# Kernel optimization log

Hardware: AMD Instinct MI355X
Metric: run time of the kernel (lower is better)

The kernel has to match this reference:

```python
import jax, jax.numpy as jnp
import numpy as np

B, S, I, H, C = 512, 512, 28, 128, 10


def setup_inputs() -> dict:
    key = jax.random.key(0)
    ks = jax.random.split(key, 11)
    std = 1.0 / np.sqrt(H)  # torch nn.RNN init scale
    u = lambda k, shape: jax.random.uniform(k, shape, jnp.float32, -std, std)
    return {
        "x": jax.random.normal(ks[0], (B, S, I), jnp.float32),
        "W_ih0": u(ks[1], (H, I)),
        "W_hh0": u(ks[2], (H, H)),
        "b_ih0": u(ks[3], (H,)),
        "b_hh0": u(ks[4], (H,)),
        "W_ih1": u(ks[5], (H, H)),
        "W_hh1": u(ks[6], (H, H)),
        "b_ih1": u(ks[7], (H,)),
        "b_hh1": u(ks[8], (H,)),
        "W_fc": u(ks[9], (C, H)),
        "b_fc": u(ks[10], (C,)),
    }


def reference(x, W_ih0, W_hh0, b_ih0, b_hh0, W_ih1, W_hh1, b_ih1, b_hh1, W_fc, b_fc):
    # 2-layer tanh RNN (batch_first); only the last timestep of layer 1 feeds fc,
    # so we carry hidden states through a scan without storing outputs.
    b = x.shape[0]
    h0_init = jnp.zeros((b, W_hh0.shape[0]), x.dtype)
    h1_init = jnp.zeros((b, W_hh1.shape[0]), x.dtype)

    def step(carry, xt):  # xt: [B, I]
        h0, h1 = carry
        h0 = jnp.tanh(xt @ W_ih0.T + b_ih0 + h0 @ W_hh0.T + b_hh0)
        h1 = jnp.tanh(h0 @ W_ih1.T + b_ih1 + h1 @ W_hh1.T + b_hh1)
        return (h0, h1), None

    xs = jnp.swapaxes(x, 0, 1)  # [S, B, I] time-major for scan
    (h0, h1), _ = jax.lax.scan(step, (h0_init, h1_init), xs)
    return h1 @ W_fc.T + b_fc  # [B, C]
```

## Files before the change

kernel.cpp:

```cpp
#include <hip/hip_runtime.h>

#define SEQ   512
#define IN    28
#define HID   128
#define NCLS  10
#define MB    16
#define PCH   144
#define MAGICF 12582912.0f

typedef __attribute__((ext_vector_type(4))) int   i32x4;
typedef __attribute__((ext_vector_type(4))) float f32x4;
typedef __attribute__((ext_vector_type(8))) short short8v;

#define SH_AA (1.0f/130048.0f)

__device__ __forceinline__ unsigned short f2bf(float f) {
    unsigned u = __float_as_uint(f);
    return (unsigned short)((u + 0x7FFFu + ((u >> 16) & 1u)) >> 16);
}
__device__ __forceinline__ float bf2f(unsigned short h) {
    return __uint_as_float(((unsigned)h) << 16);
}
__device__ __forceinline__ void split2(float f, unsigned short& hi, unsigned short& lo) {
    hi = f2bf(f);
    lo = f2bf(f - bf2f(hi));
}
__device__ __forceinline__ unsigned cvtpk(float a, float b) {
    unsigned r;
    asm("v_cvt_pk_bf16_f32 %0, %1, %2" : "=v"(r) : "v"(a), "v"(b));
    return r;
}
__device__ __forceinline__ float fast_tanh(float x) {
    float e = __expf(2.0f * x);
    return 1.0f - 2.0f * __builtin_amdgcn_rcpf(e + 1.0f);
}
__device__ __forceinline__ f32x4 mfma_bf(short8v a, short8v b, f32x4 c) {
    return __builtin_amdgcn_mfma_f32_16x16x32_bf16(a, b, c, 0, 0, 0);
}
__device__ __forceinline__ i32x4 mfma_i8(i32x4 a, i32x4 b, i32x4 c) {
    return __builtin_amdgcn_mfma_i32_16x16x64_i8(a, b, c, 0, 0, 0);
}
__device__ __forceinline__ void quantW(float wv, signed char& qa, signed char& qb) {
    int a = (int)rintf(wv * 1024.0f);
    float r = fmaf((float)a, -1.0f / 1024.0f, wv);
    int b = (int)rintf(r * 262144.0f);
    b = b > 127 ? 127 : (b < -127 ? -127 : b);
    qa = (signed char)a;
    qb = (signed char)b;
}
__device__ __forceinline__ unsigned quant4a(float t0, float t1, float t2, float t3) {
    unsigned u0 = __float_as_uint(fmaf(t0, 127.0f, MAGICF));
    unsigned u1 = __float_as_uint(fmaf(t1, 127.0f, MAGICF));
    unsigned u2 = __float_as_uint(fmaf(t2, 127.0f, MAGICF));
    unsigned u3 = __float_as_uint(fmaf(t3, 127.0f, MAGICF));
    return (u0 & 0xFFu) | ((u1 & 0xFFu) << 8) | ((u2 & 0xFFu) << 16) | ((u3 & 0xFFu) << 24);
}

union FragI8 { i32x4 v; signed char c[16]; };
union FragBF { short8v s; unsigned u[4]; };

__global__ __launch_bounds__(1024)
void rnn2_i8t(const float* __restrict__ x,
              const float* __restrict__ W_ih0, const float* __restrict__ W_hh0,
              const float* __restrict__ b_ih0, const float* __restrict__ b_hh0,
              const float* __restrict__ W_ih1, const float* __restrict__ W_hh1,
              const float* __restrict__ b_ih1, const float* __restrict__ b_hh1,
              const float* __restrict__ W_fc,  const float* __restrict__ b_fc,
              float* __restrict__ out)
{
    __shared__ __attribute__((aligned(16))) signed char hmem[2][2][MB * PCH];
    __shared__ float hfin[MB][HID + 4];

    const int t    = threadIdx.x;
    const int lane = t & 63;
    const int w    = t >> 6;
    const int lm   = lane & 15;
    const int lg   = lane >> 4;
    const int b0   = blockIdx.x * MB;
    const bool isL0 = (w < 8);
    const int T    = isL0 ? w : (w - 8);
    const int j    = 16 * T + lm;

    i32x4 Wa[2][2], Wb[2][2];
    short8v WxH = {}, WxL = {};
    float biasv[4];

    if (isL0) {
        #pragma unroll
        for (int kt = 0; kt < 2; ++kt) {
            const float* p = W_hh0 + j * HID + 64 * kt + 16 * lg;
            FragI8 a, b;
            #pragma unroll
            for (int e = 0; e < 16; ++e) quantW(p[e], a.c[e], b.c[e]);
            Wa[0][kt] = a.v; Wb[0][kt] = b.v;
        }
        FragBF H, L;
        #pragma unroll
        for (int p = 0; p < 4; ++p) {
            const int k0 = 8 * lg + 2 * p, k1 = k0 + 1;
            float w0 = (k0 < IN) ? W_ih0[j * IN + k0] : 0.0f;
            float w1 = (k1 < IN) ? W_ih0[j * IN + k1] : 0.0f;
            unsigned short h0s, l0s, h1s, l1s;
            split2(w0, h0s, l0s);
            split2(w1, h1s, l1s);
            H.u[p] = (unsigned)h0s | ((unsigned)h1s << 16);
            L.u[p] = (unsigned)l0s | ((unsigned)l1s << 16);
        }
        WxH = H.s; WxL = L.s;
        #pragma unroll
        for (int r = 0; r < 4; ++r) {
            const int u = 16 * T + 4 * lg + r;
            biasv[r] = b_ih0[u] + b_hh0[u];
        }
    } else {
        #pragma unroll
        for (int kt = 0; kt < 2; ++kt) {
            const float* p1 = W_ih1 + j * HID + 64 * kt + 16 * lg;
            const float* p2 = W_hh1 + j * HID + 64 * kt + 16 * lg;
            FragI8 a1, q1, a2, q2;
            #pragma unroll
            for (int e = 0; e < 16; ++e) {
                quantW(p1[e], a1.c[e], q1.c[e]);
                quantW(p2[e], a2.c[e], q2.c[e]);
            }
            Wa[0][kt] = a1.v; Wb[0][kt] = q1.v;
            Wa[1][kt] = a2.v; Wb[1][kt] = q2.v;
        }
        #pragma unroll
        for (int r = 0; r < 4; ++r) {
            const int u = 16 * T + 4 * lg + r;
            biasv[r] = b_ih1[u] + b_hh1[u];
        }
    }

    {
        int* z = (int*)&hmem[0][0][0];
        #pragma unroll
        for (int i = 0; i < 3; ++i) {
            const int idx = t + i * 1024;
            if (idx < (int)(sizeof(hmem) / 4)) z[idx] = 0;
        }
    }

    const float* xp = x + ((size_t)(b0 + lm) * SEQ) * IN + 8 * lg;
    float4 xA = make_float4(0.f, 0.f, 0.f, 0.f), xB = xA;
    if (isL0) {
        xA = *(const float4*)xp;
        if (lg < 3) xB = *(const float4*)(xp + 4);
    }
    __syncthreads();

    const int rbase = lm * PCH + 16 * lg;
    const int wbase = lm * PCH + 16 * T + 4 * lg;
    const i32x4 z4 = {0, 0, 0, 0};

    for (int it = 0; it <= SEQ; ++it) {
        const int rd = it & 1, wr = rd ^ 1;

        if (isL0) {
            i32x4 Ba0[2];
            Ba0[0] = *(const i32x4*)&hmem[0][rd][rbase];
            Ba0[1] = *(const i32x4*)&hmem[0][rd][rbase + 64];

            short8v BxH, BxL;
            {
                FragBF H, L;
                H.u[0] = cvtpk(xA.x, xA.y);
                H.u[1] = cvtpk(xA.z, xA.w);
                H.u[2] = cvtpk(xB.x, xB.y);
                H.u[3] = cvtpk(xB.z, xB.w);
                L.u[0] = cvtpk(xA.x - __uint_as_float(H.u[0] << 16),
                               xA.y - __uint_as_float(H.u[0] & 0xFFFF0000u));
                L.u[1] = cvtpk(xA.z - __uint_as_float(H.u[1] << 16),
                               xA.w - __uint_as_float(H.u[1] & 0xFFFF0000u));
                L.u[2] = cvtpk(xB.x - __uint_as_float(H.u[2] << 16),
                               xB.y - __uint_as_float(H.u[2] & 0xFFFF0000u));
                L.u[3] = cvtpk(xB.z - __uint_as_float(H.u[3] << 16),
                               xB.w - __uint_as_float(H.u[3] & 0xFFFF0000u));
                BxH = H.s; BxL = L.s;
            }
            {
                const int tn = (it < SEQ - 1) ? it + 1 : SEQ - 1;
                const float* p = xp + (size_t)tn * IN;
                xA = *(const float4*)p;
                xB = (lg < 3) ? *(const float4*)(p + 4) : make_float4(0.f, 0.f, 0.f, 0.f);
            }

            f32x4 accx = {biasv[0], biasv[1], biasv[2], biasv[3]};
            accx = mfma_bf(WxH, BxH, accx);
            accx = mfma_bf(WxL, BxH, accx);
            accx = mfma_bf(WxH, BxL, accx);

            i32x4 aa = mfma_i8(Wa[0][0], Ba0[0], z4);
            aa = mfma_i8(Wa[0][1], Ba0[1], aa);
            i32x4 cr = mfma_i8(Wb[0][0], Ba0[0], z4);
            cr = mfma_i8(Wb[0][1], Ba0[1], cr);

            float t0 = fast_tanh(accx[0] + SH_AA * fmaf((float)cr[0], 1.0f / 256.0f, (float)aa[0]));
            float t1 = fast_tanh(accx[1] + SH_AA * fmaf((float)cr[1], 1.0f / 256.0f, (float)aa[1]));
            float t2 = fast_tanh(accx[2] + SH_AA * fmaf((float)cr[2], 1.0f / 256.0f, (float)aa[2]));
            float t3 = fast_tanh(accx[3] + SH_AA * fmaf((float)cr[3], 1.0f / 256.0f, (float)aa[3]));
            *(unsigned*)&hmem[0][wr][wbase] = quant4a(t0, t1, t2, t3);
        } else {
            i32x4 Ba0[2], Ba1[2];
            Ba0[0] = *(const i32x4*)&hmem[0][rd][rbase];
            Ba0[1] = *(const i32x4*)&hmem[0][rd][rbase + 64];
            Ba1[0] = *(const i32x4*)&hmem[1][rd][rbase];
            Ba1[1] = *(const i32x4*)&hmem[1][rd][rbase + 64];

            i32x4 aa = mfma_i8(Wa[0][0], Ba0[0], z4);
            aa = mfma_i8(Wa[0][1], Ba0[1], aa);
            aa = mfma_i8(Wa[1][0], Ba1[0], aa);
            aa = mfma_i8(Wa[1][1], Ba1[1], aa);
            i32x4 cr = mfma_i8(Wb[0][0], Ba0[0], z4);
            cr = mfma_i8(Wb[0][1], Ba0[1], cr);
            cr = mfma_i8(Wb[1][0], Ba1[0], cr);
            cr = mfma_i8(Wb[1][1], Ba1[1], cr);

            float t0, t1, t2, t3;
            if (it == 0) {
                t0 = t1 = t2 = t3 = 0.0f;
            } else {
                t0 = fast_tanh(biasv[0] + SH_AA * fmaf((float)cr[0], 1.0f / 256.0f, (float)aa[0]));
                t1 = fast_tanh(biasv[1] + SH_AA * fmaf((float)cr[1], 1.0f / 256.0f, (float)aa[1]));
                t2 = fast_tanh(biasv[2] + SH_AA * fmaf((float)cr[2], 1.0f / 256.0f, (float)aa[2]));
                t3 = fast_tanh(biasv[3] + SH_AA * fmaf((float)cr[3], 1.0f / 256.0f, (float)aa[3]));
            }
            *(unsigned*)&hmem[1][wr][wbase] = quant4a(t0, t1, t2, t3);
            if (it == SEQ) {
                const int u = 16 * T + 4 * lg;
                hfin[lm][u + 0] = t0;
                hfin[lm][u + 1] = t1;
                hfin[lm][u + 2] = t2;
                hfin[lm][u + 3] = t3;
            }
        }
        __syncthreads();
    }

    if (t < MB * NCLS) {
        const int r = t / NCLS, c = t % NCLS;
        float acc = b_fc[c];
        const float* hf = &hfin[r][0];
        #pragma unroll 4
        for (int k = 0; k < HID; ++k)
            acc = fmaf(W_fc[c * HID + k], hf[k], acc);
        out[(b0 + r) * NCLS + c] = acc;
    }
}

extern "C" void kernel_launch(void* const* d_in, const int* in_sizes, int n_in,
                              void* d_out, int out_size, void* d_ws, size_t ws_size,
                              hipStream_t stream) {
    const float* x     = (const float*)d_in[0];
    const float* W_ih0 = (const float*)d_in[1];
    const float* W_hh0 = (const float*)d_in[2];
    const float* b_ih0 = (const float*)d_in[3];
    const float* b_hh0 = (const float*)d_in[4];
    const float* W_ih1 = (const float*)d_in[5];
    const float* W_hh1 = (const float*)d_in[6];
    const float* b_ih1 = (const float*)d_in[7];
    const float* b_hh1 = (const float*)d_in[8];
    const float* W_fc  = (const float*)d_in[9];
    const float* b_fc  = (const float*)d_in[10];
    float* out = (float*)d_out;

    rnn2_i8t<<<dim3(512 / MB), dim3(1024), 0, stream>>>(
        x, W_ih0, W_hh0, b_ih0, b_hh0, W_ih1, W_hh1, b_ih1, b_hh1, W_fc, b_fc, out);
}
```

Baseline: 329.4 us.

## Rebalance layer-1 waves to two tiles each and drop bf16 low-part input MFMAs

Layer 1 now runs on 4 waves that each compute two 16-row output tiles, so the block shrinks from 16 to 12 waves and per-wave layer-1 work matches layer-0's critical path more closely. The input projection keeps only the bf16 high part of x and W_ih0, removing two of three MFMAs and the split conversions. This trades input-projection precision for fewer instructions. Smaller tweaks fold the integer recombination into one shift-add plus fma, use exp2 in tanh, and pack bytes with v_perm.

Result: slower. 375.1 us (+13.9%).

```diff
diff --git a/kernel.cpp b/kernel.cpp
--- a/kernel.cpp
+++ b/kernel.cpp
@@ -12,18 +12,11 @@
 typedef __attribute__((ext_vector_type(4))) float f32x4;
 typedef __attribute__((ext_vector_type(8))) short short8v;
 
-#define SH_AA (1.0f/130048.0f)
+#define SH_CR (1.0f/33292288.0f)
 
 __device__ __forceinline__ unsigned short f2bf(float f) {
     unsigned u = __float_as_uint(f);
     return (unsigned short)((u + 0x7FFFu + ((u >> 16) & 1u)) >> 16);
-}
-__device__ __forceinline__ float bf2f(unsigned short h) {
-    return __uint_as_float(((unsigned)h) << 16);
-}
-__device__ __forceinline__ void split2(float f, unsigned short& hi, unsigned short& lo) {
-    hi = f2bf(f);
-    lo = f2bf(f - bf2f(hi));
 }
 __device__ __forceinline__ unsigned cvtpk(float a, float b) {
     unsigned r;
@@ -31,7 +24,7 @@
     return r;
 }
 __device__ __forceinline__ float fast_tanh(float x) {
-    float e = __expf(2.0f * x);
+    float e = exp2f(x * 2.8853900817779268f);
     return 1.0f - 2.0f * __builtin_amdgcn_rcpf(e + 1.0f);
 }
 __device__ __forceinline__ f32x4 mfma_bf(short8v a, short8v b, f32x4 c) {
@@ -53,14 +46,16 @@
     unsigned u1 = __float_as_uint(fmaf(t1, 127.0f, MAGICF));
     unsigned u2 = __float_as_uint(fmaf(t2, 127.0f, MAGICF));
     unsigned u3 = __float_as_uint(fmaf(t3, 127.0f, MAGICF));
-    return (u0 & 0xFFu) | ((u1 & 0xFFu) << 8) | ((u2 & 0xFFu) << 16) | ((u3 & 0xFFu) << 24);
+    unsigned t01 = __builtin_amdgcn_perm(u1, u0, 0x00000400u);
+    unsigned t23 = __builtin_amdgcn_perm(u3, u2, 0x00000400u);
+    return __builtin_amdgcn_perm(t23, t01, 0x05040100u);
 }
 
 union FragI8 { i32x4 v; signed char c[16]; };
 union FragBF { short8v s; unsigned u[4]; };
 
-__global__ __launch_bounds__(1024)
-void rnn2_i8t(const float* __restrict__ x,
+__global__ __launch_bounds__(768)
+void rnn2_i8w(const float* __restrict__ x,
               const float* __restrict__ W_ih0, const float* __restrict__ W_hh0,
               const float* __restrict__ b_ih0, const float* __restrict__ b_hh0,
               const float* __restrict__ W_ih1, const float* __restrict__ W_hh1,
@@ -78,14 +73,16 @@
     const int lg   = lane >> 4;
     const int b0   = blockIdx.x * MB;
     const bool isL0 = (w < 8);
-    const int T    = isL0 ? w : (w - 8);
-    const int j    = 16 * T + lm;
 
     i32x4 Wa[2][2], Wb[2][2];
-    short8v WxH = {}, WxL = {};
-    float biasv[4];
+    i32x4 W1a[2][2], W1b[2][2];
+    i32x4 W2a[2][2], W2b[2][2];
+    short8v WxH = {};
+    float bias0v[4];
+    float bias1v[2][4];
 
     if (isL0) {
+        const int j = 16 * w + lm;
         #pragma unroll
         for (int kt = 0; kt < 2; ++kt) {
             const float* p = W_hh0 + j * HID + 64 * kt + 16 * lg;
@@ -94,52 +91,51 @@
             for (int e = 0; e < 16; ++e) quantW(p[e], a.c[e], b.c[e]);
             Wa[0][kt] = a.v; Wb[0][kt] = b.v;
         }
-        FragBF H, L;
+        FragBF H;
         #pragma unroll
         for (int p = 0; p < 4; ++p) {
             const int k0 = 8 * lg + 2 * p, k1 = k0 + 1;
             float w0 = (k0 < IN) ? W_ih0[j * IN + k0] : 0.0f;
             float w1 = (k1 < IN) ? W_ih0[j * IN + k1] : 0.0f;
-            unsigned short h0s, l0s, h1s, l1s;
-            split2(w0, h0s, l0s);
-            split2(w1, h1s, l1s);
-            H.u[p] = (unsigned)h0s | ((unsigned)h1s << 16);
-            L.u[p] = (unsigned)l0s | ((unsigned)l1s << 16);
-        }
-        WxH = H.s; WxL = L.s;
+            H.u[p] = (unsigned)f2bf(w0) | ((unsigned)f2bf(w1) << 16);
+        }
+        WxH = H.s;
         #pragma unroll
         for (int r = 0; r < 4; ++r) {
-            const int u = 16 * T + 4 * lg + r;
-            biasv[r] = b_ih0[u] + b_hh0[u];
+            const int u = 16 * w + 4 * lg + r;
+            bias0v[r] = b_ih0[u] + b_hh0[u];
         }
     } else {
-        #pragma unroll
-        for (int kt = 0; kt < 2; ++kt) {
-            const float* p1 = W_ih1 + j * HID + 64 * kt + 16 * lg;
-            const float* p2 = W_hh1 + j * HID + 64 * kt + 16 * lg;
-            FragI8 a1, q1, a2, q2;
-            #pragma unroll
-            for (int e = 0; e < 16; ++e) {
-                quantW(p1[e], a1.c[e], q1.c[e]);
-                quantW(p2[e], a2.c[e], q2.c[e]);
-            }
-            Wa[0][kt] = a1.v; Wb[0][kt] = q1.v;
-            Wa[1][kt] = a2.v; Wb[1][kt] = q2.v;
-        }
-        #pragma unroll
-        for (int r = 0; r < 4; ++r) {
-            const int u = 16 * T + 4 * lg + r;
-            biasv[r] = b_ih1[u] + b_hh1[u];
+        const int w1 = w - 8;
+        #pragma unroll
+        for (int tile = 0; tile < 2; ++tile) {
+            const int T = 2 * w1 + tile;
+            const int j = 16 * T + lm;
+            #pragma unroll
+            for (int kt = 0; kt < 2; ++kt) {
+                const float* p1 = W_ih1 + j * HID + 64 * kt + 16 * lg;
+                const float* p2 = W_hh1 + j * HID + 64 * kt + 16 * lg;
+                FragI8 a1, q1, a2, q2;
+                #pragma unroll
+                for (int e = 0; e < 16; ++e) {
+                    quantW(p1[e], a1.c[e], q1.c[e]);
+                    quantW(p2[e], a2.c[e], q2.c[e]);
+                }
+                W1a[tile][kt] = a1.v; W1b[tile][kt] = q1.v;
+                W2a[tile][kt] = a2.v; W2b[tile][kt] = q2.v;
+            }
+            #pragma unroll
+            for (int r = 0; r < 4; ++r) {
+                const int u = 16 * T + 4 * lg + r;
+                bias1v[tile][r] = b_ih1[u] + b_hh1[u];
+            }
         }
     }
 
     {
         int* z = (int*)&hmem[0][0][0];
         #pragma unroll
-        for (int i = 0; i < 3; ++i) {
-            const int idx = t + i * 1024;
-            if (idx < (int)(sizeof(hmem) / 4)) z[idx] = 0;
-        }
+        for (int i = 0; i < 3; ++i) z[t + i * 768] = 0;
     }
 
     const float* xp = x + ((size_t)(b0 + lm) * SEQ) * IN + 8 * lg;
@@ -151,7 +147,6 @@
     __syncthreads();
 
     const int rbase = lm * PCH + 16 * lg;
-    const int wbase = lm * PCH + 16 * T + 4 * lg;
     const i32x4 z4 = {0, 0, 0, 0};
 
     for (int it = 0; it <= SEQ; ++it) {
@@ -162,23 +157,11 @@
             Ba0[0] = *(const i32x4*)&hmem[0][rd][rbase];
             Ba0[1] = *(const i32x4*)&hmem[0][rd][rbase + 64];
 
-            short8v BxH, BxL;
-            {
-                FragBF H, L;
-                H.u[0] = cvtpk(xA.x, xA.y);
-                H.u[1] = cvtpk(xA.z, xA.w);
-                H.u[2] = cvtpk(xB.x, xB.y);
-                H.u[3] = cvtpk(xB.z, xB.w);
-                L.u[0] = cvtpk(xA.x - __uint_as_float(H.u[0] << 16),
-                               xA.y - __uint_as_float(H.u[0] & 0xFFFF0000u));
-                L.u[1] = cvtpk(xA.z - __uint_as_float(H.u[1] << 16),
-                               xA.w - __uint_as_float(H.u[1] & 0xFFFF0000u));
-                L.u[2] = cvtpk(xB.x - __uint_as_float(H.u[2] << 16),
-                               xB.y - __uint_as_float(H.u[2] & 0xFFFF0000u));
-                L.u[3] = cvtpk(xB.z - __uint_as_float(H.u[3] << 16),
-                               xB.w - __uint_as_float(H.u[3] & 0xFFFF0000u));
-                BxH = H.s; BxL = L.s;
-            }
+            FragBF H;
+            H.u[0] = cvtpk(xA.x, xA.y);
+            H.u[1] = cvtpk(xA.z, xA.w);
+            H.u[2] = cvtpk(xB.x, xB.y);
+            H.u[3] = cvtpk(xB.z, xB.w);
             {
                 const int tn = (it < SEQ - 1) ? it + 1 : SEQ - 1;
                 const float* p = xp + (size_t)tn * IN;
@@ -186,21 +169,20 @@
                 xB = (lg < 3) ? *(const float4*)(p + 4) : make_float4(0.f, 0.f, 0.f, 0.f);
             }
 
-            f32x4 accx = {biasv[0], biasv[1], biasv[2], biasv[3]};
-            accx = mfma_bf(WxH, BxH, accx);
-            accx = mfma_bf(WxL, BxH, accx);
-            accx = mfma_bf(WxH, BxL, accx);
+            f32x4 accx = {bias0v[0], bias0v[1], bias0v[2], bias0v[3]};
+            accx = mfma_bf(WxH, H.s, accx);
 
             i32x4 aa = mfma_i8(Wa[0][0], Ba0[0], z4);
             aa = mfma_i8(Wa[0][1], Ba0[1], aa);
             i32x4 cr = mfma_i8(Wb[0][0], Ba0[0], z4);
             cr = mfma_i8(Wb[0][1], Ba0[1], cr);
 
-            float t0 = fast_tanh(accx[0] + SH_AA * fmaf((float)cr[0], 1.0f / 256.0f, (float)aa[0]));
-            float t1 = fast_tanh(accx[1] + SH_AA * fmaf((float)cr[1], 1.0f / 256.0f, (float)aa[1]));
-            float t2 = fast_tanh(accx[2] + SH_AA * fmaf((float)cr[2], 1.0f / 256.0f, (float)aa[2]));
-            float t3 = fast_tanh(accx[3] + SH_AA * fmaf((float)cr[3], 1.0f / 256.0f, (float)aa[3]));
-            *(unsigned*)&hmem[0][wr][wbase] = quant4a(t0, t1, t2, t3);
+            float t0 = fast_tanh(fmaf((float)((aa[0] << 8) + cr[0]), SH_CR, accx[0]));
+            float t1 = fast_tanh(fmaf((float)((aa[1] << 8) + cr[1]), SH_CR, accx[1]));
+            float t2 = fast_tanh(fmaf((float)((aa[2] << 8) + cr[2]), SH_CR, accx[2]));
+            float t3 = fast_tanh(fmaf((float)((aa[3] << 8) + cr[3]), SH_CR, accx[3]));
+            const int wb = lm * PCH + 16 * w + 4 * lg;
+            *(unsigned*)&hmem[0][wr][wb] = quant4a(t0, t1, t2, t3);
         } else {
             i32x4 Ba0[2], Ba1[2];
             Ba0[0] = *(const i32x4*)&hmem[0][rd][rbase];
@@ -208,31 +190,37 @@
             Ba1[0] = *(const i32x4*)&hmem[1][rd][rbase];
             Ba1[1] = *(const i32x4*)&hmem[1][rd][rbase + 64];
 
-            i32x4 aa = mfma_i8(Wa[0][0], Ba0[0], z4);
-            aa = mfma_i8(Wa[0][1], Ba0[1], aa);
-            aa = mfma_i8(Wa[1][0], Ba1[0], aa);
-            aa = mfma_i8(Wa[1][1], Ba1[1], aa);
-            i32x4 cr = mfma_i8(Wb[0][0], Ba0[0], z4);
-            cr = mfma_i8(Wb[0][1], Ba0[1], cr);
-            cr = mfma_i8(Wb[1][0], Ba1[0], cr);
-            cr = mfma_i8(Wb[1][1], Ba1[1], cr);
-
-            float t0, t1, t2, t3;
-            if (it == 0) {
-                t0 = t1 = t2 = t3 = 0.0f;
-            } else {
-                t0 = fast_tanh(biasv[0] + SH_AA * fmaf((float)cr[0], 1.0f / 256.0f, (float)aa[0]));
-                t1 = fast_tanh(biasv[1] + SH_AA * fmaf((float)cr[1], 1.0f / 256.0f, (float)aa[1]));
-                t2 = fast_tanh(biasv[2] + SH_AA * fmaf((float)cr[2], 1.0f / 256.0f, (float)aa[2]));
-                t3 = fast_tanh(biasv[3] + SH_AA * fmaf((float)cr[3], 1.0f / 256.0f, (float)aa[3]));
-            }
-            *(unsigned*)&hmem[1][wr][wbase] = quant4a(t0, t1, t2, t3);
-            if (it == SEQ) {
-                const int u = 16 * T + 4 * lg;
-                hfin[lm][u + 0] = t0;
-                hfin[lm][u + 1] = t1;
-                hfin[lm][u + 2] = t2;
-                hfin[lm][u + 3] = t3;
+            const int w1 = w - 8;
+            #pragma unroll
+            for (int tile = 0; tile < 2; ++tile) {
+                i32x4 aa = mfma_i8(W1a[tile][0], Ba0[0], z4);
+                aa = mfma_i8(W1a[tile][1], Ba0[1], aa);
+                aa = mfma_i8(W2a[tile][0], Ba1[0], aa);
+                aa = mfma_i8(W2a[tile][1], Ba1[1], aa);
+                i32x4 cr = mfma_i8(W1b[tile][0], Ba0[0], z4);
+                cr = mfma_i8(W1b[tile][1], Ba0[1], cr);
+                cr = mfma_i8(W2b[tile][0], Ba1[0], cr);
+                cr = mfma_i8(W2b[tile][1], Ba1[1], cr);
+
+                float t0, t1, t2, t3;
+                if (it == 0) {
+                    t0 = t1 = t2 = t3 = 0.0f;
+                } else {
+                    t0 = fast_tanh(fmaf((float)((aa[0] << 8) + cr[0]), SH_CR, bias1v[tile][0]));
+                    t1 = fast_tanh(fmaf((float)((aa[1] << 8) + cr[1]), SH_CR, bias1v[tile][1]));
+                    t2 = fast_tanh(fmaf((float)((aa[2] << 8) + cr[2]), SH_CR, bias1v[tile][2]));
+                    t3 = fast_tanh(fmaf((float)((aa[3] << 8) + cr[3]), SH_CR, bias1v[tile][3]));
+                }
+                const int T = 2 * w1 + tile;
+                const int wb = lm * PCH + 16 * T + 4 * lg;
+                *(unsigned*)&hmem[1][wr][wb] = quant4a(t0, t1, t2, t3);
+                if (it == SEQ) {
+                    const int u = 16 * T + 4 * lg;
+                    hfin[lm][u + 0] = t0;
+                    hfin[lm][u + 1] = t1;
+                    hfin[lm][u + 2] = t2;
+                    hfin[lm][u + 3] = t3;
+                }
             }
         }
         __syncthreads();
@@ -265,6 +253,6 @@
     const float* b_fc  = (const float*)d_in[10];
     float* out = (float*)d_out;
 
-    rnn2_i8t<<<dim3(512 / MB), dim3(1024), 0, stream>>>(
+    rnn2_i8w<<<dim3(512 / MB), dim3(768), 0, stream>>>(
         x, W_ih0, W_hh0, b_ih0, b_hh0, W_ih1, W_hh1, b_ih1, b_hh1, W_fc, b_fc, out);
 }
```
